# Optimization experiments

Hardware: AMD Instinct MI355X
Metric: run time of the kernel (lower is better)

The kernel has to match this reference:

```python
import jax, jax.numpy as jnp
import numpy as np

B, S, DIM, HDIM = 8, 1024, 1024, 128
H = DIM // HDIM  # 8 heads
GN_EPS = 1e-3    # keras GroupNormalization default epsilon


def group_norm(y, gamma, beta, groups, eps=GN_EPS):
    # keras GroupNormalization on [B,S,C]: reshape to [B,S,groups,C//groups],
    # normalize over all axes except batch and group axis -> axes (1,3).
    b, s, c = y.shape
    g = y.reshape(b, s, groups, c // groups)
    mean = g.mean(axis=(1, 3), keepdims=True)
    var = g.var(axis=(1, 3), keepdims=True)
    g = (g - mean) * jax.lax.rsqrt(var + eps)
    return g.reshape(b, s, c) * gamma + beta


def setup_inputs() -> dict:
    key = jax.random.key(0)
    ks = jax.random.split(key, 7)
    x = jax.random.normal(ks[0], (B, S, DIM), dtype=jnp.float32)
    sc_h = 1.0 / np.sqrt(HDIM).astype(np.float32)
    sc_d = 1.0 / np.sqrt(DIM).astype(np.float32)
    Wq = jax.random.normal(ks[1], (H, HDIM, HDIM), dtype=jnp.float32) * sc_h
    Wk = jax.random.normal(ks[2], (H, HDIM, HDIM), dtype=jnp.float32) * sc_h
    Wv = jax.random.normal(ks[3], (H, HDIM, HDIM), dtype=jnp.float32) * sc_h
    Wg = jax.random.normal(ks[4], (DIM, DIM), dtype=jnp.float32) * sc_d
    Wo = jax.random.normal(ks[5], (DIM, DIM), dtype=jnp.float32) * sc_d
    gn_gamma = jnp.ones((DIM,), dtype=jnp.float32)
    gn_beta = jnp.zeros((DIM,), dtype=jnp.float32)
    return {"x": x, "Wq": Wq, "Wk": Wk, "Wv": Wv, "Wg": Wg, "Wo": Wo,
            "gn_gamma": gn_gamma, "gn_beta": gn_beta}


def reference(x, Wq, Wk, Wv, Wg, Wo, gn_gamma, gn_beta):
    b, s, c = x.shape
    h, hd = Wq.shape[0], Wq.shape[1]
    # gating branch: W = ReLU(x @ Wg)
    Wgate = jax.nn.relu(jnp.einsum('bsc,cd->bsd', x, Wg))
    # split channels into heads: [B,S,H,hd]
    xh = x.reshape(b, s, h, hd)
    Q = jnp.einsum('bshd,hde->bhse', xh, Wq)
    K = jnp.einsum('bshd,hde->bhse', xh, Wk)
    V = jnp.einsum('bshd,hde->bhse', xh, Wv)
    # per-head decay mask D[h,i,j] = gamma_h ** (i - j) (full, non-causal as in source)
    idx = jnp.arange(s, dtype=jnp.float32)
    gammas = 1.0 - 2.0 ** (-5.0 - jnp.arange(h, dtype=jnp.float32))  # [H]
    decay = gammas[:, None, None] ** (idx[None, :, None] - idx[None, None, :])  # [H,S,S]
    scores = jnp.einsum('bhsd,bhtd->bhst', Q, K) * decay[None]
    ret = jnp.einsum('bhst,bhtd->bhsd', scores, V)       # [B,H,S,hd]
    y = ret.transpose(0, 2, 1, 3).reshape(b, s, c)        # concat heads
    Y = group_norm(y, gn_gamma, gn_beta, groups=hd)       # groups = hdim (keras arg)
    return jnp.einsum('bsc,cd->bsd', Wgate * Y, Wo)
```

## Files before the change

### kernel.cpp

```cpp
#include <hip/hip_runtime.h>

#define BB 8
#define SS 1024
#define DD 1024
#define HH 8
#define HD 128
#define GN_EPS 1e-3f

typedef __attribute__((ext_vector_type(8))) short bf16x8;
typedef __attribute__((ext_vector_type(4))) float f32x4;

__device__ __forceinline__ short f2bf(float f) {
    unsigned u = __float_as_uint(f);
    return (short)((u + 0x7fffu + ((u >> 16) & 1u)) >> 16);
}
__device__ __forceinline__ float bf2f(short s) {
    return __uint_as_float(((unsigned)(unsigned short)s) << 16);
}

__device__ __forceinline__ void gload16(const void* g, void* l) {
    __builtin_amdgcn_global_load_lds((const __attribute__((address_space(1))) void*)g,
                                     (__attribute__((address_space(3))) void*)l, 16, 0, 0);
}

__device__ __forceinline__ void stage_tile(const short* __restrict__ G, size_t ld, int k0,
                                           short* lds, int wid, int lane) {
#pragma unroll
    for (int i = 0; i < 2; i++) {
        const int seg = wid * 2 + i;
        const int row = seg * 8 + (lane >> 3);
        const int chunk = (lane & 7) ^ (lane >> 3);
        gload16(G + (size_t)row * ld + k0 + chunk * 8, lds + seg * 512);
    }
}

__device__ __forceinline__ void gemm_tile_g(
    const short* __restrict__ A, size_t ldA,
    const short* __restrict__ B, size_t ldB,
    int K, short* As, short* Bs, f32x4 acc[4][2])
{
    const int tid = threadIdx.x, lane = tid & 63, wid = tid >> 6;
    const int wr = (wid >> 2) * 64, wc = (wid & 3) * 32;
    const int fr = lane & 15, fc = lane >> 4;
    const int rsw = fr & 7;
#pragma unroll
    for (int i = 0; i < 4; i++)
#pragma unroll
        for (int j = 0; j < 2; j++) acc[i][j] = (f32x4){0.f, 0.f, 0.f, 0.f};

    const int nt = K >> 6;
    stage_tile(A, ldA, 0, As, wid, lane);
    stage_tile(B, ldB, 0, Bs, wid, lane);
    if (nt > 1) {
        stage_tile(A, ldA, 64, As + 8192, wid, lane);
        stage_tile(B, ldB, 64, Bs + 8192, wid, lane);
    }
    for (int t = 0; t < nt; t++) {
        if (t + 1 < nt) asm volatile("s_waitcnt vmcnt(4)" ::: "memory");
        else            asm volatile("s_waitcnt vmcnt(0)" ::: "memory");
        __builtin_amdgcn_s_barrier();
        __builtin_amdgcn_sched_barrier(0);
        const int cur = t & 1;
        const short* as = As + (cur << 13);
        const short* bs = Bs + (cur << 13);
#pragma unroll
        for (int half = 0; half < 2; half++) {
            const int slot = ((half * 4 + fc) ^ rsw) << 3;
            bf16x8 af[4], bfv[2];
#pragma unroll
            for (int i = 0; i < 4; i++) af[i] = *(const bf16x8*)&as[(wr + i * 16 + fr) * 64 + slot];
#pragma unroll
            for (int j = 0; j < 2; j++) bfv[j] = *(const bf16x8*)&bs[(wc + j * 16 + fr) * 64 + slot];
#pragma unroll
            for (int i = 0; i < 4; i++)
#pragma unroll
                for (int j = 0; j < 2; j++)
                    acc[i][j] = __builtin_amdgcn_mfma_f32_16x16x32_bf16(af[i], bfv[j], acc[i][j], 0, 0, 0);
        }
        __builtin_amdgcn_sched_barrier(0);
        asm volatile("s_waitcnt lgkmcnt(0)" ::: "memory");
        __builtin_amdgcn_s_barrier();
        if (t + 2 < nt) {
            stage_tile(A, ldA, (t + 2) << 6, As + (cur << 13), wid, lane);
            stage_tile(B, ldB, (t + 2) << 6, Bs + (cur << 13), wid, lane);
        }
    }
}

__global__ __launch_bounds__(256) void prep(
    const float* __restrict__ x,
    const float* __restrict__ Wq, const float* __restrict__ Wk, const float* __restrict__ Wv,
    const float* __restrict__ Wg, const float* __restrict__ Wo,
    short* __restrict__ xb, short* __restrict__ WgT, short* __restrict__ WoT,
    short* __restrict__ Wt, float* __restrict__ sQ, float* __restrict__ sK,
    float* __restrict__ Sp)
{
    __shared__ float t[32][33];
    int bid = blockIdx.x;
    const int tid = threadIdx.x;
    if (bid < 4096) {
        const size_t i = ((size_t)bid * 256 + tid) * 8;
        float4 a = *(const float4*)&x[i];
        float4 b = *(const float4*)&x[i + 4];
        bf16x8 v;
        v[0] = f2bf(a.x); v[1] = f2bf(a.y); v[2] = f2bf(a.z); v[3] = f2bf(a.w);
        v[4] = f2bf(b.x); v[5] = f2bf(b.y); v[6] = f2bf(b.z); v[7] = f2bf(b.w);
        *(bf16x8*)&xb[i] = v;
        return;
    }
    bid -= 4096;
    if (bid < 2048) {
        const float* __restrict__ S = (bid < 1024) ? Wg : Wo;
        short* __restrict__ D = (bid < 1024) ? WgT : WoT;
        const int tb = bid & 1023;
        const int bx = (tb & 31) * 32, by = (tb >> 5) * 32;
        const int xx = tid & 31, y0 = tid >> 5;
#pragma unroll
        for (int r = 0; r < 32; r += 8) t[y0 + r][xx] = S[(size_t)(by + y0 + r) * 1024 + bx + xx];
        __syncthreads();
#pragma unroll
        for (int r = 0; r < 32; r += 8) D[(size_t)(bx + y0 + r) * 1024 + by + xx] = f2bf(t[xx][y0 + r]);
        return;
    }
    bid -= 2048;
    if (bid < 384) {
        const int ht = bid >> 4, tb = bid & 15;
        const int typ = ht >> 3, h = ht & 7;
        const float* __restrict__ W = (typ == 0 ? Wq : (typ == 1 ? Wk : Wv)) + (size_t)h * HD * HD;
        short* __restrict__ D = Wt + (size_t)ht * HD * HD;
        const int bx = (tb & 3) * 32, by = (tb >> 2) * 32;
        const int xx = tid & 31, y0 = tid >> 5;
#pragma unroll
        for (int r = 0; r < 32; r += 8) t[y0 + r][xx] = W[(by + y0 + r) * HD + bx + xx];
        __syncthreads();
#pragma unroll
        for (int r = 0; r < 32; r += 8) D[(bx + y0 + r) * HD + by + xx] = f2bf(t[xx][y0 + r]);
        return;
    }
    bid -= 384;
    if (bid < 32) {
        const int h = bid >> 2;
        const int s = (bid & 3) * 256 + tid;
        const double gamma = 1.0 - exp2((double)(-5 - h));
        const double lg = log2(gamma);
        sQ[h * SS + s] = (float)exp2(lg * (double)s);
        sK[h * SS + s] = (float)exp2(-lg * (double)s);
        return;
    }
    *(float4*)&Sp[tid * 8] = (float4){0.f, 0.f, 0.f, 0.f};
    *(float4*)&Sp[tid * 8 + 4] = (float4){0.f, 0.f, 0.f, 0.f};
}

__global__ __launch_bounds__(512) void g_qkvgate(
    const short* __restrict__ xb, const short* __restrict__ Wt, const short* __restrict__ WgT,
    const float* __restrict__ sQ, const float* __restrict__ sK,
    short* __restrict__ Qb, short* __restrict__ Ktb, short* __restrict__ Vtb,
    short* __restrict__ gateb)
{
    __shared__ short As[2 * 8192], Bs[2 * 8192];
    f32x4 acc[4][2];
    const int orig = blockIdx.x;
    const int cx = orig & 7, p = orig >> 3;
    const int tid = threadIdx.x, lane = tid & 63, wid = tid >> 6;
    const int wr = (wid >> 2) * 64, wc = (wid & 3) * 32;
    const int r0 = (lane >> 4) * 4, c = lane & 15;

    if (p < 64) {
        const int w2 = cx * 64 + p;
        const int m0 = (w2 >> 3) * 128, n0 = (w2 & 7) * 128;
        gemm_tile_g(xb + (size_t)m0 * DD, DD, WgT + (size_t)n0 * DD, DD, DD, As, Bs, acc);
#pragma unroll
        for (int i = 0; i < 4; i++)
#pragma unroll
            for (int j = 0; j < 2; j++)
#pragma unroll
                for (int r = 0; r < 4; r++)
                    gateb[(size_t)(m0 + wr + i * 16 + r0 + r) * DD + n0 + wc + j * 16 + c] =
                        f2bf(fmaxf(acc[i][j][r], 0.f));
        return;
    }
    const int w = cx * 64 + (p - 64);
    const int mt = w >> 3, h = w & 7;
    const int m0 = mt * 128;
    const int b = m0 >> 10, s0 = m0 & (SS - 1);
    const int bh = (b << 3) + h;
    const short* __restrict__ A = xb + (size_t)m0 * DD + h * HD;

    const int fr = lane & 15, fc = lane >> 4;
    const int rsw = fr & 7;

    stage_tile(A, DD, 0,  As,        wid, lane);
    stage_tile(A, DD, 64, As + 8192, wid, lane);
    stage_tile(Wt + (size_t)h * HD * HD, HD, 0,  Bs,        wid, lane);
    stage_tile(Wt + (size_t)h * HD * HD, HD, 64, Bs + 8192, wid, lane);

#pragma unroll
    for (int i = 0; i < 4; i++)
#pragma unroll
        for (int j = 0; j < 2; j++) acc[i][j] = (f32x4){0.f, 0.f, 0.f, 0.f};

    for (int st = 0; st < 6; st++) {
        if (st + 1 < 6) asm volatile("s_waitcnt vmcnt(2)" ::: "memory");
        else            asm volatile("s_waitcnt vmcnt(0)" ::: "memory");
        __builtin_amdgcn_s_barrier();
        __builtin_amdgcn_sched_barrier(0);
        const int kt = st & 1;
        const short* as = As + (kt << 13);
        const short* bs = Bs + (kt << 13);
#pragma unroll
        for (int half = 0; half < 2; half++) {
            const int slot = ((half * 4 + fc) ^ rsw) << 3;
            bf16x8 af[4], bfv[2];
#pragma unroll
            for (int i = 0; i < 4; i++) af[i] = *(const bf16x8*)&as[(wr + i * 16 + fr) * 64 + slot];
#pragma unroll
            for (int j = 0; j < 2; j++) bfv[j] = *(const bf16x8*)&bs[(wc + j * 16 + fr) * 64 + slot];
#pragma unroll
            for (int i = 0; i < 4; i++)
#pragma unroll
                for (int j = 0; j < 2; j++)
                    acc[i][j] = __builtin_amdgcn_mfma_f32_16x16x32_bf16(af[i], bfv[j], acc[i][j], 0, 0, 0);
        }
        __builtin_amdgcn_sched_barrier(0);
        asm volatile("s_waitcnt lgkmcnt(0)" ::: "memory");
        __builtin_amdgcn_s_barrier();
        if (kt == 1) {
            const int typ = st >> 1;
            if (typ == 0) {
#pragma unroll
                for (int i = 0; i < 4; i++)
#pragma unroll
                    for (int j = 0; j < 2; j++)
#pragma unroll
                        for (int r = 0; r < 4; r++) {
                            const int s = s0 + wr + i * 16 + r0 + r;
                            Qb[((size_t)bh * SS + s) * HD + wc + j * 16 + c] =
                                f2bf(acc[i][j][r] * sQ[h * SS + s]);
                        }
            } else if (typ == 1) {
                short* __restrict__ Ob = Ktb + (size_t)bh * HD * SS;
#pragma unroll
                for (int i = 0; i < 4; i++)
#pragma unroll
                    for (int j = 0; j < 2; j++) {
                        const int tb = s0 + wr + i * 16 + r0;
                        const int d = wc + j * 16 + c;
                        short4 o;
                        o.x = f2bf(acc[i][j][0] * sK[h * SS + tb + 0]);
                        o.y = f2bf(acc[i][j][1] * sK[h * SS + tb + 1]);
                        o.z = f2bf(acc[i][j][2] * sK[h * SS + tb + 2]);
                        o.w = f2bf(acc[i][j][3] * sK[h * SS + tb + 3]);
                        *(short4*)&Ob[(size_t)d * SS + tb] = o;
                    }
            } else {
                short* __restrict__ Ob = Vtb + (size_t)bh * HD * SS;
#pragma unroll
                for (int i = 0; i < 4; i++)
#pragma unroll
                    for (int j = 0; j < 2; j++) {
                        const int tb = s0 + wr + i * 16 + r0;
                        const int e = wc + j * 16 + c;
                        short4 o;
                        o.x = f2bf(acc[i][j][0]); o.y = f2bf(acc[i][j][1]);
                        o.z = f2bf(acc[i][j][2]); o.w = f2bf(acc[i][j][3]);
                        *(short4*)&Ob[(size_t)e * SS + tb] = o;
                    }
            }
#pragma unroll
            for (int i = 0; i < 4; i++)
#pragma unroll
                for (int j = 0; j < 2; j++) acc[i][j] = (f32x4){0.f, 0.f, 0.f, 0.f};
        }
        __builtin_amdgcn_sched_barrier(0);
        if (st + 2 < 6) {
            const int typn = (st + 2) >> 1, ktn = (st + 2) & 1;
            stage_tile(Wt + (size_t)(typn * 8 + h) * HD * HD, HD, ktn * 64,
                       Bs + (kt << 13), wid, lane);
        }
    }
}

__global__ __launch_bounds__(512) void g_kv(
    const short* __restrict__ Vtb, const short* __restrict__ Ktb, float* __restrict__ Mp)
{
    __shared__ short As[2 * 8192], Bs[2 * 8192];
    f32x4 acc[4][2];
    const int orig = blockIdx.x;
    const int w = (orig & 7) * 16 + (orig >> 3);
    const int chunk = w & 1, bh = w >> 1;
    gemm_tile_g(Vtb + (size_t)bh * HD * SS + chunk * 512, SS,
                Ktb + (size_t)bh * HD * SS + chunk * 512, SS, 512, As, Bs, acc);
    const int tid = threadIdx.x, lane = tid & 63, wid = tid >> 6;
    const int wr = (wid >> 2) * 64, wc = (wid & 3) * 32;
    const int r0 = (lane >> 4) * 4, c = lane & 15;
    float* __restrict__ Ob = Mp + (size_t)w * HD * HD;
#pragma unroll
    for (int i = 0; i < 4; i++)
#pragma unroll
        for (int j = 0; j < 2; j++)
#pragma unroll
            for (int r = 0; r < 4; r++)
                Ob[(size_t)(wr + i * 16 + r0 + r) * HD + wc + j * 16 + c] = acc[i][j][r];
}

__global__ __launch_bounds__(256) void g_mredcvt(const float* __restrict__ Mp, short* __restrict__ Mtb) {
    const size_t i = ((size_t)blockIdx.x * 256 + threadIdx.x) * 8;
    const size_t bh = i >> 14, ij = i & 16383;
    const float* p = Mp + (bh * 2) * 16384 + ij;
    float s[8];
#pragma unroll
    for (int q = 0; q < 8; q++) s[q] = 0.f;
#pragma unroll
    for (int cth = 0; cth < 2; cth++) {
        float4 a = *(const float4*)&p[cth * 16384];
        float4 b = *(const float4*)&p[cth * 16384 + 4];
        s[0] += a.x; s[1] += a.y; s[2] += a.z; s[3] += a.w;
        s[4] += b.x; s[5] += b.y; s[6] += b.z; s[7] += b.w;
    }
    bf16x8 v;
#pragma unroll
    for (int q = 0; q < 8; q++) v[q] = f2bf(s[q]);
    *(bf16x8*)&Mtb[i] = v;
}

__global__ __launch_bounds__(512) void g_qm(
    const short* __restrict__ Qb, const short* __restrict__ Mtb,
    short* __restrict__ retc, float* __restrict__ Sp)
{
    __shared__ short As[2 * 8192], Bs[2 * 8192];
    f32x4 acc[4][2];
    const int orig = blockIdx.x;
    const int w = (orig & 7) * 64 + (orig >> 3);
    const int bh = w >> 3, m0 = (w & 7) * 128;
    const short* __restrict__ A = Qb + ((size_t)bh * SS + m0) * HD;
    const short* __restrict__ Bp = Mtb + (size_t)bh * HD * HD;
    const int tid = threadIdx.x, lane = tid & 63, wid = tid >> 6;
    const int wr = (wid >> 2) * 64, wc = (wid & 3) * 32;
    const int fr = lane & 15, fc = lane >> 4, rsw = fr & 7;
    const int r0 = (lane >> 4) * 4, c = lane & 15;

    stage_tile(A,  HD, 0,  As,        wid, lane);
    stage_tile(A,  HD, 64, As + 8192, wid, lane);
    stage_tile(Bp, HD, 0,  Bs,        wid, lane);
    stage_tile(Bp, HD, 64, Bs + 8192, wid, lane);
#pragma unroll
    for (int i = 0; i < 4; i++)
#pragma unroll
        for (int j = 0; j < 2; j++) acc[i][j] = (f32x4){0.f, 0.f, 0.f, 0.f};
    asm volatile("s_waitcnt vmcnt(0)" ::: "memory");
    __builtin_amdgcn_s_barrier();
    __builtin_amdgcn_sched_barrier(0);
#pragma unroll
    for (int kt = 0; kt < 2; kt++) {
        const short* as = As + (kt << 13);
        const short* bs = Bs + (kt << 13);
#pragma unroll
        for (int half = 0; half < 2; half++) {
            const int slot = ((half * 4 + fc) ^ rsw) << 3;
            bf16x8 af[4], bfv[2];
#pragma unroll
            for (int i = 0; i < 4; i++) af[i] = *(const bf16x8*)&as[(wr + i * 16 + fr) * 64 + slot];
#pragma unroll
            for (int j = 0; j < 2; j++) bfv[j] = *(const bf16x8*)&bs[(wc + j * 16 + fr) * 64 + slot];
#pragma unroll
            for (int i = 0; i < 4; i++)
#pragma unroll
                for (int j = 0; j < 2; j++)
                    acc[i][j] = __builtin_amdgcn_mfma_f32_16x16x32_bf16(af[i], bfv[j], acc[i][j], 0, 0, 0);
        }
    }
    const int b_ = bh >> 3, h_ = bh & 7;
    short* __restrict__ O = retc + ((size_t)(b_ * SS + m0)) * DD + h_ * HD;
#pragma unroll
    for (int i = 0; i < 4; i++)
#pragma unroll
        for (int j = 0; j < 2; j++)
#pragma unroll
            for (int r = 0; r < 4; r++)
                O[(size_t)(wr + i * 16 + r0 + r) * DD + wc + j * 16 + c] = f2bf(acc[i][j][r]);

    float psm[2], psq[2];
#pragma unroll
    for (int j = 0; j < 2; j++) { psm[j] = 0.f; psq[j] = 0.f; }
#pragma unroll
    for (int i = 0; i < 4; i++)
#pragma unroll
        for (int j = 0; j < 2; j++)
#pragma unroll
            for (int r = 0; r < 4; r++) {
                const float v = acc[i][j][r];
                psm[j] += v; psq[j] += v * v;
            }
    const int masks[5] = {1, 2, 4, 16, 32};
#pragma unroll
    for (int mk = 0; mk < 5; mk++) {
#pragma unroll
        for (int j = 0; j < 2; j++) {
            psm[j] += __shfl_xor(psm[j], masks[mk], 64);
            psq[j] += __shfl_xor(psq[j], masks[mk], 64);
        }
    }
    if ((lane & 7) == 0 && lane < 16) {
        const int hi = lane >> 3;
#pragma unroll
        for (int j = 0; j < 2; j++) {
            const int g = b_ * 128 + h_ * 16 + (wid & 3) * 4 + j * 2 + hi;
            atomicAdd(&Sp[g * 2 + 0], psm[j]);
            atomicAdd(&Sp[g * 2 + 1], psq[j]);
        }
    }
}

__global__ __launch_bounds__(256) void aprep(
    const short* __restrict__ gateb, const short* __restrict__ retc,
    const float* __restrict__ Sp,
    const float* __restrict__ gng, const float* __restrict__ gnb, short* __restrict__ Ab)
{
    const size_t idx = ((size_t)blockIdx.x * 256 + threadIdx.x) * 4;
    const int m = (int)(idx >> 10), cc = (int)(idx & 1023);
    const int b_ = m >> 10, g = b_ * 128 + (cc >> 3);
    const float sm = Sp[g * 2 + 0], sq = Sp[g * 2 + 1];
    const float mu = sm * (1.0f / 8192.0f);
    float var = sq * (1.0f / 8192.0f) - mu * mu;
    if (var < 0.f) var = 0.f;
    const float rs = rsqrtf(var + GN_EPS);
    short4 gv4 = *(const short4*)&gateb[idx];
    short4 rv4 = *(const short4*)&retc[idx];
    float4 gv = *(const float4*)&gng[cc];
    float4 bv = *(const float4*)&gnb[cc];
    short4 o;
    o.x = f2bf(bf2f(gv4.x) * ((bf2f(rv4.x) - mu) * rs * gv.x + bv.x));
    o.y = f2bf(bf2f(gv4.y) * ((bf2f(rv4.y) - mu) * rs * gv.y + bv.y));
    o.z = f2bf(bf2f(gv4.z) * ((bf2f(rv4.z) - mu) * rs * gv.z + bv.z));
    o.w = f2bf(bf2f(gv4.w) * ((bf2f(rv4.w) - mu) * rs * gv.w + bv.w));
    *(short4*)&Ab[idx] = o;
}

__global__ __launch_bounds__(512) void g_final(
    const short* __restrict__ Ab, const short* __restrict__ WoT, float* __restrict__ out)
{
    __shared__ short As[2 * 8192], Bs[2 * 8192];
    f32x4 acc[4][2];
    const int orig = blockIdx.x;
    const int w = (orig & 7) * 64 + (orig >> 3);
    const int m0 = (w >> 3) * 128, n0 = (w & 7) * 128;
    gemm_tile_g(Ab + (size_t)m0 * DD, DD, WoT + (size_t)n0 * DD, DD, DD, As, Bs, acc);
    const int tid = threadIdx.x, lane = tid & 63, wid = tid >> 6;
    const int wr = (wid >> 2) * 64, wc = (wid & 3) * 32;
    const int r0 = (lane >> 4) * 4, c = lane & 15;
#pragma unroll
    for (int i = 0; i < 4; i++)
#pragma unroll
        for (int j = 0; j < 2; j++)
#pragma unroll
            for (int r = 0; r < 4; r++)
                out[(size_t)(m0 + wr + i * 16 + r0 + r) * DD + n0 + wc + j * 16 + c] = acc[i][j][r];
}

extern "C" void kernel_launch(void* const* d_in, const int* in_sizes, int n_in,
                              void* d_out, int out_size, void* d_ws, size_t ws_size,
                              hipStream_t stream)
{
    const float* x   = (const float*)d_in[0];
    const float* Wq  = (const float*)d_in[1];
    const float* Wk  = (const float*)d_in[2];
    const float* Wv  = (const float*)d_in[3];
    const float* Wg  = (const float*)d_in[4];
    const float* Wo  = (const float*)d_in[5];
    const float* gng = (const float*)d_in[6];
    const float* gnb = (const float*)d_in[7];
    float* out = (float*)d_out;

    char* ws = (char*)d_ws;
    size_t off = 0;
    auto alloc = [&](size_t bytes) -> void* {
        void* p = ws + off;
        off += (bytes + 255) & ~(size_t)255;
        return p;
    };
    const size_t NE = (size_t)BB * SS * DD;
    float*  sQ    = (float*)alloc((size_t)HH * SS * sizeof(float));
    float*  sK    = (float*)alloc((size_t)HH * SS * sizeof(float));
    short*  xb    = (short*)alloc(NE * sizeof(short));
    short*  WgT   = (short*)alloc((size_t)DD * DD * sizeof(short));
    short*  WoT   = (short*)alloc((size_t)DD * DD * sizeof(short));
    short*  Wt    = (short*)alloc((size_t)24 * HD * HD * sizeof(short));
    short*  Qb    = (short*)alloc(NE * sizeof(short));
    short*  Ktb   = (short*)alloc(NE * sizeof(short));
    short*  Vtb   = (short*)alloc(NE * sizeof(short));
    short*  retc  = (short*)alloc(NE * sizeof(short));
    short*  gateb = (short*)alloc(NE * sizeof(short));
    short*  Ab    = (short*)alloc(NE * sizeof(short));
    float*  Mp    = (float*)alloc((size_t)128 * HD * HD * sizeof(float));
    short*  Mtb   = (short*)alloc((size_t)64 * HD * HD * sizeof(short));
    float*  Sp    = (float*)alloc((size_t)1024 * 2 * sizeof(float));

    prep<<<dim3(6561), 256, 0, stream>>>(x, Wq, Wk, Wv, Wg, Wo, xb, WgT, WoT, Wt, sQ, sK, Sp);
    g_qkvgate<<<dim3(1024), 512, 0, stream>>>(xb, Wt, WgT, sQ, sK, Qb, Ktb, Vtb, gateb);
    g_kv<<<dim3(128), 512, 0, stream>>>(Vtb, Ktb, Mp);
    g_mredcvt<<<dim3(512), 256, 0, stream>>>(Mp, Mtb);
    g_qm<<<dim3(512), 512, 0, stream>>>(Qb, Mtb, retc, Sp);
    aprep<<<dim3(8192), 256, 0, stream>>>(gateb, retc, Sp, gng, gnb, Ab);
    g_final<<<dim3(512), 512, 0, stream>>>(Ab, WoT, out);
}
```

Measured before the change: 112.5 us.

## Use 256x128 ping-pong GEMM tiles for gate and output projections

```diff
diff --git a/kernel.cpp b/kernel.cpp
--- a/kernel.cpp
+++ b/kernel.cpp
@@ -28,6 +28,17 @@
 #pragma unroll
     for (int i = 0; i < 2; i++) {
         const int seg = wid * 2 + i;
+        const int row = seg * 8 + (lane >> 3);
+        const int chunk = (lane & 7) ^ (lane >> 3);
+        gload16(G + (size_t)row * ld + k0 + chunk * 8, lds + seg * 512);
+    }
+}
+
+__device__ __forceinline__ void stage_A256_part(const short* __restrict__ G, size_t ld, int k0,
+                                                short* lds, int wid, int lane, int part) {
+#pragma unroll
+    for (int i = 0; i < 2; i++) {
+        const int seg = wid * 4 + part * 2 + i;
         const int row = seg * 8 + (lane >> 3);
         const int chunk = (lane & 7) ^ (lane >> 3);
         gload16(G + (size_t)row * ld + k0 + chunk * 8, lds + seg * 512);
@@ -84,6 +95,69 @@
             stage_tile(A, ldA, (t + 2) << 6, As + (cur << 13), wid, lane);
             stage_tile(B, ldB, (t + 2) << 6, Bs + (cur << 13), wid, lane);
         }
+    }
+}
+
+__device__ __forceinline__ void gemm_tile_p(
+    const short* __restrict__ A, size_t ldA,
+    const short* __restrict__ B, size_t ldB,
+    int K, short* As, short* Bs, f32x4 acc[4][4])
+{
+    const int tid = threadIdx.x, lane = tid & 63, wid = tid >> 6;
+    const int wr = (wid >> 1) * 64, wc = (wid & 1) * 64;
+    const int fr = lane & 15, fc = lane >> 4;
+    const int rsw = fr & 7;
+#pragma unroll
+    for (int i = 0; i < 4; i++)
+#pragma unroll
+        for (int j = 0; j < 4; j++) acc[i][j] = (f32x4){0.f, 0.f, 0.f, 0.f};
+
+    const int nt = K >> 6;
+    stage_A256_part(A, ldA, 0, As, wid, lane, 0);
+    stage_A256_part(A, ldA, 0, As, wid, lane, 1);
+    stage_tile(B, ldB, 0, Bs, wid, lane);
+    asm volatile("s_waitcnt vmcnt(0)" ::: "memory");
+    __builtin_amdgcn_s_barrier();
+
+    int cur = 0;
+    for (int t = 0; t < nt; t++) {
+        const short* as = As + (cur << 14);
+        const short* bs = Bs + (cur << 13);
+        short* asn = As + ((cur ^ 1) << 14);
+        short* bsn = Bs + ((cur ^ 1) << 13);
+#pragma unroll
+        for (int half = 0; half < 2; half++) {
+            const int slot = ((half * 4 + fc) ^ rsw) << 3;
+            bf16x8 af[4], bfv[4];
+#pragma unroll
+            for (int i = 0; i < 4; i++) af[i] = *(const bf16x8*)&as[(wr + i * 16 + fr) * 64 + slot];
+#pragma unroll
+            for (int j = 0; j < 4; j++) bfv[j] = *(const bf16x8*)&bs[(wc + j * 16 + fr) * 64 + slot];
+            if (t + 1 < nt) {
+                if (half == 0) {
+                    stage_A256_part(A, ldA, (t + 1) << 6, asn, wid, lane, 0);
+                } else {
+                    stage_A256_part(A, ldA, (t + 1) << 6, asn, wid, lane, 1);
+                    stage_tile(B, ldB, (t + 1) << 6, bsn, wid, lane);
+                }
+            }
+            __builtin_amdgcn_s_barrier();
+            asm volatile("s_waitcnt lgkmcnt(0)" ::: "memory");
+            __builtin_amdgcn_sched_barrier(0);
+            __builtin_amdgcn_s_setprio(1);
+#pragma unroll
+            for (int i = 0; i < 4; i++)
+#pragma unroll
+                for (int j = 0; j < 4; j++)
+                    acc[i][j] = __builtin_amdgcn_mfma_f32_16x16x32_bf16(af[i], bfv[j], acc[i][j], 0, 0, 0);
+            __builtin_amdgcn_s_setprio(0);
+            __builtin_amdgcn_s_barrier();
+        }
+        if (t + 1 < nt) {
+            asm volatile("s_waitcnt vmcnt(0)" ::: "memory");
+            __builtin_amdgcn_s_barrier();
+        }
+        cur ^= 1;
     }
 }
 
@@ -151,41 +225,23 @@
     *(float4*)&Sp[tid * 8 + 4] = (float4){0.f, 0.f, 0.f, 0.f};
 }
 
-__global__ __launch_bounds__(512) void g_qkvgate(
-    const short* __restrict__ xb, const short* __restrict__ Wt, const short* __restrict__ WgT,
+__global__ __launch_bounds__(512) void g_qkv(
+    const short* __restrict__ xb, const short* __restrict__ Wt,
     const float* __restrict__ sQ, const float* __restrict__ sK,
-    short* __restrict__ Qb, short* __restrict__ Ktb, short* __restrict__ Vtb,
-    short* __restrict__ gateb)
+    short* __restrict__ Qb, short* __restrict__ Ktb, short* __restrict__ Vtb)
 {
     __shared__ short As[2 * 8192], Bs[2 * 8192];
     f32x4 acc[4][2];
     const int orig = blockIdx.x;
-    const int cx = orig & 7, p = orig >> 3;
-    const int tid = threadIdx.x, lane = tid & 63, wid = tid >> 6;
-    const int wr = (wid >> 2) * 64, wc = (wid & 3) * 32;
-    const int r0 = (lane >> 4) * 4, c = lane & 15;
-
-    if (p < 64) {
-        const int w2 = cx * 64 + p;
-        const int m0 = (w2 >> 3) * 128, n0 = (w2 & 7) * 128;
-        gemm_tile_g(xb + (size_t)m0 * DD, DD, WgT + (size_t)n0 * DD, DD, DD, As, Bs, acc);
-#pragma unroll
-        for (int i = 0; i < 4; i++)
-#pragma unroll
-            for (int j = 0; j < 2; j++)
-#pragma unroll
-                for (int r = 0; r < 4; r++)
-                    gateb[(size_t)(m0 + wr + i * 16 + r0 + r) * DD + n0 + wc + j * 16 + c] =
-                        f2bf(fmaxf(acc[i][j][r], 0.f));
-        return;
-    }
-    const int w = cx * 64 + (p - 64);
+    const int w = (orig & 7) * 64 + (orig >> 3);
     const int mt = w >> 3, h = w & 7;
     const int m0 = mt * 128;
     const int b = m0 >> 10, s0 = m0 & (SS - 1);
     const int bh = (b << 3) + h;
     const short* __restrict__ A = xb + (size_t)m0 * DD + h * HD;
-
+    const int tid = threadIdx.x, lane = tid & 63, wid = tid >> 6;
+    const int wr = (wid >> 2) * 64, wc = (wid & 3) * 32;
+    const int r0 = (lane >> 4) * 4, c = lane & 15;
     const int fr = lane & 15, fc = lane >> 4;
     const int rsw = fr & 7;
 
@@ -278,6 +334,28 @@
                        Bs + (kt << 13), wid, lane);
         }
     }
+}
+
+__global__ __launch_bounds__(512) void g_gate(
+    const short* __restrict__ xb, const short* __restrict__ WgT, short* __restrict__ gateb)
+{
+    __shared__ short As[2 * 16384], Bs[2 * 8192];
+    f32x4 acc[4][4];
+    const int orig = blockIdx.x;
+    const int w = (orig & 7) * 32 + (orig >> 3);
+    const int m0 = (w >> 3) * 256, n0 = (w & 7) * 128;
+    gemm_tile_p(xb + (size_t)m0 * DD, DD, WgT + (size_t)n0 * DD, DD, DD, As, Bs, acc);
+    const int tid = threadIdx.x, lane = tid & 63, wid = tid >> 6;
+    const int wr = (wid >> 1) * 64, wc = (wid & 1) * 64;
+    const int r0 = (lane >> 4) * 4, c = lane & 15;
+#pragma unroll
+    for (int i = 0; i < 4; i++)
+#pragma unroll
+        for (int j = 0; j < 4; j++)
+#pragma unroll
+            for (int r = 0; r < 4; r++)
+                gateb[(size_t)(m0 + wr + i * 16 + r0 + r) * DD + n0 + wc + j * 16 + c] =
+                    f2bf(fmaxf(acc[i][j][r], 0.f));
 }
 
 __global__ __launch_bounds__(512) void g_kv(
@@ -439,19 +517,19 @@
 __global__ __launch_bounds__(512) void g_final(
     const short* __restrict__ Ab, const short* __restrict__ WoT, float* __restrict__ out)
 {
-    __shared__ short As[2 * 8192], Bs[2 * 8192];
-    f32x4 acc[4][2];
+    __shared__ short As[2 * 16384], Bs[2 * 8192];
+    f32x4 acc[4][4];
     const int orig = blockIdx.x;
-    const int w = (orig & 7) * 64 + (orig >> 3);
-    const int m0 = (w >> 3) * 128, n0 = (w & 7) * 128;
-    gemm_tile_g(Ab + (size_t)m0 * DD, DD, WoT + (size_t)n0 * DD, DD, DD, As, Bs, acc);
-    const int tid = threadIdx.x, lane = tid & 63, wid = tid >> 6;
-    const int wr = (wid >> 2) * 64, wc = (wid & 3) * 32;
+    const int w = (orig & 7) * 32 + (orig >> 3);
+    const int m0 = (w >> 3) * 256, n0 = (w & 7) * 128;
+    gemm_tile_p(Ab + (size_t)m0 * DD, DD, WoT + (size_t)n0 * DD, DD, DD, As, Bs, acc);
+    const int tid = threadIdx.x, lane = tid & 63, wid = tid >> 6;
+    const int wr = (wid >> 1) * 64, wc = (wid & 1) * 64;
     const int r0 = (lane >> 4) * 4, c = lane & 15;
 #pragma unroll
     for (int i = 0; i < 4; i++)
 #pragma unroll
-        for (int j = 0; j < 2; j++)
+        for (int j = 0; j < 4; j++)
 #pragma unroll
             for (int r = 0; r < 4; r++)
                 out[(size_t)(m0 + wr + i * 16 + r0 + r) * DD + n0 + wc + j * 16 + c] = acc[i][j][r];
@@ -496,10 +574,11 @@
     float*  Sp    = (float*)alloc((size_t)1024 * 2 * sizeof(float));
 
     prep<<<dim3(6561), 256, 0, stream>>>(x, Wq, Wk, Wv, Wg, Wo, xb, WgT, WoT, Wt, sQ, sK, Sp);
-    g_qkvgate<<<dim3(1024), 512, 0, stream>>>(xb, Wt, WgT, sQ, sK, Qb, Ktb, Vtb, gateb);
+    g_qkv<<<dim3(512), 512, 0, stream>>>(xb, Wt, sQ, sK, Qb, Ktb, Vtb);
+    g_gate<<<dim3(256), 512, 0, stream>>>(xb, WgT, gateb);
     g_kv<<<dim3(128), 512, 0, stream>>>(Vtb, Ktb, Mp);
     g_mredcvt<<<dim3(512), 256, 0, stream>>>(Mp, Mtb);
     g_qm<<<dim3(512), 512, 0, stream>>>(Qb, Mtb, retc, Sp);
     aprep<<<dim3(8192), 256, 0, stream>>>(gateb, retc, Sp, gng, gnb, Ab);
-    g_final<<<dim3(512), 512, 0, stream>>>(Ab, WoT, out);
-}
+    g_final<<<dim3(256), 512, 0, stream>>>(Ab, WoT, out);
+}
```

Result: slower. 120.4 us (+7.1%).
